# Kernel optimization log

Measured on AMD Instinct MI355X. Metric: run time of the kernel, lower is better.

Reference implementation:

```python
import jax, jax.numpy as jnp
import numpy as np

EPS = 1e-6


def _layernorm2d(x, w, b):
    # Normalize over channel dim (axis=1) per pixel; x: [B,C,H,W]
    mu = jnp.mean(x, axis=1, keepdims=True)
    var = jnp.var(x, axis=1, keepdims=True)
    xn = (x - mu) * jax.lax.rsqrt(var + EPS)
    return xn * w[None, :, None, None] + b[None, :, None, None]


def _conv1x1(x, w, b):
    # 1x1 conv == channel matmul; w: [Cout, Cin], x: [B,Cin,H,W]
    return jnp.einsum('oc,bchw->bohw', w, x) + b[None, :, None, None]


def setup_inputs() -> dict:
    key = jax.random.key(0)
    ks = jax.random.split(key, 8)
    B, C, H, W = 4, 64, 180, 320
    s = C ** -0.5  # keep projection weights at sane scale
    return {
        'x_l': jax.random.normal(ks[0], (B, C, H, W), jnp.float32),
        'x_r': jax.random.normal(ks[1], (B, C, H, W), jnp.float32),
        'ln_l_w': jnp.ones((C,), jnp.float32),
        'ln_l_b': jnp.zeros((C,), jnp.float32),
        'ln_r_w': jnp.ones((C,), jnp.float32),
        'ln_r_b': jnp.zeros((C,), jnp.float32),
        'wq_l': jax.random.normal(ks[2], (C, C), jnp.float32) * s,
        'bq_l': jnp.zeros((C,), jnp.float32),
        'wq_r': jax.random.normal(ks[3], (C, C), jnp.float32) * s,
        'bq_r': jnp.zeros((C,), jnp.float32),
        'wv_l': jax.random.normal(ks[4], (C, C), jnp.float32) * s,
        'bv_l': jnp.zeros((C,), jnp.float32),
        'wv_r': jax.random.normal(ks[5], (C, C), jnp.float32) * s,
        'bv_r': jnp.zeros((C,), jnp.float32),
        'beta': jax.random.normal(ks[6], (C,), jnp.float32) * 0.1,
        'gamma': jax.random.normal(ks[7], (C,), jnp.float32) * 0.1,
    }


def reference(x_l, x_r, ln_l_w, ln_l_b, ln_r_w, ln_r_b,
              wq_l, bq_l, wq_r, bq_r, wv_l, bv_l, wv_r, bv_r,
              beta, gamma):
    C = x_l.shape[1]
    scale = C ** -0.5
    # Q projections of LayerNorm'd inputs (Select stub == identity pass-through)
    Q_l = _conv1x1(_layernorm2d(x_l, ln_l_w, ln_l_b), wq_l, bq_l)  # [B,C,H,W]
    Q_r = _conv1x1(_layernorm2d(x_r, ln_r_w, ln_r_b), wq_r, bq_r)  # [B,C,H,W]
    V_l = _conv1x1(x_l, wv_l, bv_l)  # [B,C,H,W]
    V_r = _conv1x1(x_r, wv_r, bv_r)  # [B,C,H,W]
    # attention over width per row: [B,H,Wl,Wr]
    attn = jnp.einsum('bchw,bchv->bhwv', Q_l, Q_r) * scale
    # r -> l: softmax over Wr (last axis), contract with V_r
    F_r2l = jnp.einsum('bhwv,bchv->bchw', jax.nn.softmax(attn, axis=-1), V_r)
    # l -> r: softmax over Wl (axis=2 of attn), contract with V_l
    F_l2r = jnp.einsum('bhwv,bchw->bchv', jax.nn.softmax(attn, axis=2), V_l)
    out_l = x_l + F_r2l * beta[None, :, None, None]
    out_r = x_r + F_l2r * gamma[None, :, None, None]
    return (out_l, out_r)
```

## Files before the change

### kernel.cpp

```cpp
#include <hip/hip_runtime.h>


#define HWs  57600
#define CHWs 3686400
#define TOTs 14745600
#define RST  72
#define VST  328
#define PTS  36
#define NTH  768

typedef short bf16x8 __attribute__((ext_vector_type(8)));
typedef float f32x4  __attribute__((ext_vector_type(4)));
union FragU { uint4 q; unsigned short u[8]; bf16x8 v; };

__device__ __forceinline__ unsigned short f2bf(float f) {
  unsigned u = __float_as_uint(f);
  u += 0x7fffu + ((u >> 16) & 1u);
  return (unsigned short)(u >> 16);
}
__device__ __forceinline__ float bf2f(unsigned short s) {
  return __uint_as_float(((unsigned)s) << 16);
}
__device__ __forceinline__ unsigned fenc(float f) {
  unsigned u = __float_as_uint(f);
  return u ^ (0x80000000u | (unsigned)(-(int)(u >> 31)));
}
__device__ __forceinline__ float fdec(unsigned k) {
  return __uint_as_float(k ^ (0x80000000u | (unsigned)(-(int)((k >> 31) ^ 1u))));
}

__global__ __launch_bounds__(NTH, 3)
void sfam_kernel(
    const float* __restrict__ x_l, const float* __restrict__ x_r,
    const float* __restrict__ ln_l_w, const float* __restrict__ ln_l_b,
    const float* __restrict__ ln_r_w, const float* __restrict__ ln_r_b,
    const float* __restrict__ wq_l, const float* __restrict__ bq_l,
    const float* __restrict__ wq_r, const float* __restrict__ bq_r,
    const float* __restrict__ wv_l, const float* __restrict__ bv_l,
    const float* __restrict__ wv_r, const float* __restrict__ bv_r,
    const float* __restrict__ beta, const float* __restrict__ gamma,
    float* __restrict__ out)
{
  __shared__ __align__(16) unsigned short Rs[320*RST];
  __shared__ __align__(16) unsigned short Ks[320*RST];
  __shared__ __align__(16) unsigned short Vb[64*VST];
  __shared__ __align__(16) unsigned short Pt[12*16*PTS];
  __shared__ unsigned CMu[320];
  __shared__ float MU[640], RSd[640];
  __shared__ float c_arr[320];
  __shared__ float BB[128];

  const int bh = blockIdx.x;
  const int b = bh / 180, h = bh - b*180;
  const int base = b*CHWs + h*320;

  const int t = threadIdx.x;
  const int wave = t >> 6, lane = t & 63;
  const int p = lane & 15, g = lane >> 4;
  const int nwt = (wave < 8) ? 2 : 1;
  const int w0 = (wave < 8) ? wave*32 : 256 + (wave-8)*16;

  for (int w2 = t; w2 < 640; w2 += NTH) {
    const int side = (w2 >= 320);
    const int w = w2 - side*320;
    const float* xp = side ? x_r : x_l;
    unsigned short* dst = side ? Ks : Rs;
    float s0 = 0.f, q0 = 0.f, s1 = 0.f, q1 = 0.f;
    #pragma unroll
    for (int cb = 0; cb < 64; cb += 8) {
      FragU f;
      #pragma unroll
      for (int j = 0; j < 8; ++j) {
        const float v = xp[base + (cb+j)*HWs + w];
        if (cb < 32) { s0 += v; q0 += v*v; } else { s1 += v; q1 += v*v; }
        f.u[j] = f2bf(v);
      }
      *(uint4*)&dst[w*RST + cb] = f.q;
    }
    const float m  = (s0 + s1) * (1.f/64.f);
    const float vv = (q0 + q1) * (1.f/64.f) - m*m;
    MU[side*320 + w]  = m;
    RSd[side*320 + w] = rsqrtf(vv + 1e-6f);
  }
  if (t < 320) CMu[t] = 0u;
  if (t < 128) {
    const int o = t & 63;
    const float* wqp = (t < 64) ? wq_l : wq_r;
    const float* lwp = (t < 64) ? ln_l_w : ln_r_w;
    const float* lbp = (t < 64) ? ln_l_b : ln_r_b;
    const float* bqp = (t < 64) ? bq_l : bq_r;
    float s = bqp[o];
    for (int c = 0; c < 64; ++c) s += wqp[o*64+c]*lwp[c]*lbp[c];
    BB[t] = s;
  }
  __syncthreads();

  auto projV = [&](const float* wvp, const float* bvp, const unsigned short* src,
                   const float* mup, const float* rsp, bool inv) {
    bf16x8 bx[2][2];
    #pragma unroll
    for (int nt = 0; nt < 2; ++nt) if (nt < nwt) {
      const int w = w0 + nt*16 + p;
      const float mu = mup[w];
      const float sd = inv ? (1.0f / rsp[w]) : 0.f;
      #pragma unroll
      for (int kf = 0; kf < 2; ++kf) {
        FragU f; f.q = *(const uint4*)&src[w*RST + kf*32 + g*8];
        if (inv) {
          FragU rr;
          #pragma unroll
          for (int j = 0; j < 8; ++j) rr.u[j] = f2bf(bf2f(f.u[j])*sd + mu);
          bx[nt][kf] = rr.v;
        } else bx[nt][kf] = f.v;
      }
    }
    bf16x8 av[4][2];
    #pragma unroll
    for (int mt = 0; mt < 4; ++mt)
      #pragma unroll
      for (int kf = 0; kf < 2; ++kf) {
        FragU rr;
        #pragma unroll
        for (int j = 0; j < 8; ++j) rr.u[j] = f2bf(wvp[(mt*16+p)*64 + kf*32 + g*8 + j]);
        av[mt][kf] = rr.v;
      }
    f32x4 acc[4][2];
    #pragma unroll
    for (int mt = 0; mt < 4; ++mt)
      #pragma unroll
      for (int nt = 0; nt < 2; ++nt) acc[mt][nt] = (f32x4){0.f,0.f,0.f,0.f};
    #pragma unroll
    for (int mt = 0; mt < 4; ++mt)
      #pragma unroll
      for (int nt = 0; nt < 2; ++nt) if (nt < nwt)
        #pragma unroll
        for (int kf = 0; kf < 2; ++kf)
          acc[mt][nt] = __builtin_amdgcn_mfma_f32_16x16x32_bf16(av[mt][kf], bx[nt][kf], acc[mt][nt], 0,0,0);
    #pragma unroll
    for (int mt = 0; mt < 4; ++mt)
      #pragma unroll
      for (int nt = 0; nt < 2; ++nt) if (nt < nwt)
        #pragma unroll
        for (int r = 0; r < 4; ++r) {
          const int o = mt*16 + g*4 + r;
          Vb[o*VST + w0 + nt*16 + p] = f2bf(acc[mt][nt][r] + bvp[o]);
        }
  };

  projV(wv_l, bv_l, Rs, MU, RSd, false);

  float cR[2][4];
  {
    bf16x8 qa[2][2];
    #pragma unroll
    for (int wt = 0; wt < 2; ++wt) if (wt < nwt) {
      const int w = w0 + wt*16 + p;
      const float mu = MU[w], rs = RSd[w];
      #pragma unroll
      for (int kf = 0; kf < 2; ++kf) {
        FragU f; f.q = *(const uint4*)&Rs[w*RST + kf*32 + g*8];
        FragU rr;
        #pragma unroll
        for (int j = 0; j < 8; ++j) rr.u[j] = f2bf((bf2f(f.u[j]) - mu) * rs);
        qa[wt][kf] = rr.v;
      }
    }
    bf16x8 bw[4][2];
    #pragma unroll
    for (int ot = 0; ot < 4; ++ot)
      #pragma unroll
      for (int kf = 0; kf < 2; ++kf) {
        FragU rr;
        #pragma unroll
        for (int j = 0; j < 8; ++j) {
          const int c = kf*32 + g*8 + j;
          rr.u[j] = f2bf(wq_l[(ot*16+p)*64 + c] * ln_l_w[c]);
        }
        bw[ot][kf] = rr.v;
      }
    f32x4 qacc[2][4];
    #pragma unroll
    for (int wt = 0; wt < 2; ++wt)
      #pragma unroll
      for (int ot = 0; ot < 4; ++ot) qacc[wt][ot] = (f32x4){0.f,0.f,0.f,0.f};
    #pragma unroll
    for (int wt = 0; wt < 2; ++wt) if (wt < nwt)
      #pragma unroll
      for (int ot = 0; ot < 4; ++ot)
        #pragma unroll
        for (int kf = 0; kf < 2; ++kf)
          qacc[wt][ot] = __builtin_amdgcn_mfma_f32_16x16x32_bf16(qa[wt][kf], bw[ot][kf], qacc[wt][ot], 0,0,0);
    #pragma unroll
    for (int wt = 0; wt < 2; ++wt) {
      #pragma unroll
      for (int r = 0; r < 4; ++r) cR[wt][r] = 0.f;
      if (wt < nwt) {
        #pragma unroll
        for (int ot = 0; ot < 4; ++ot) {
          const float bl = BB[ot*16+p], br = BB[64 + ot*16+p];
          #pragma unroll
          for (int r = 0; r < 4; ++r) {
            const float qv = qacc[wt][ot][r] + bl;
            Rs[(w0 + wt*16 + g*4 + r)*RST + ot*16 + p] = f2bf(qv);
            cR[wt][r] += qv * br;
          }
        }
        #pragma unroll
        for (int r = 0; r < 4; ++r) {
          float cv = cR[wt][r];
          cv += __shfl_xor(cv, 1); cv += __shfl_xor(cv, 2);
          cv += __shfl_xor(cv, 4); cv += __shfl_xor(cv, 8);
          cv *= 0.125f;
          cR[wt][r] = cv;
          if (p == 0) c_arr[w0 + wt*16 + g*4 + r] = cv;
        }
      }
    }
  }

  {
    bf16x8 qla[2][2];
    #pragma unroll
    for (int wt = 0; wt < 2; ++wt) if (wt < nwt)
      #pragma unroll
      for (int kf = 0; kf < 2; ++kf) {
        FragU f; f.q = *(const uint4*)&Rs[(w0 + wt*16 + p)*RST + kf*32 + g*8];
        qla[wt][kf] = f.v;
      }
    bf16x8 bwt[4][2];
    #pragma unroll
    for (int ct = 0; ct < 4; ++ct) {
      const float lw = ln_r_w[ct*16 + p];
      #pragma unroll
      for (int kf = 0; kf < 2; ++kf) {
        FragU rr;
        #pragma unroll
        for (int j = 0; j < 8; ++j)
          rr.u[j] = f2bf(wq_r[(kf*32 + g*8 + j)*64 + ct*16 + p] * lw);
        bwt[ct][kf] = rr.v;
      }
    }
    f32x4 q2[2][4];
    #pragma unroll
    for (int wt = 0; wt < 2; ++wt)
      #pragma unroll
      for (int ct = 0; ct < 4; ++ct) q2[wt][ct] = (f32x4){0.f,0.f,0.f,0.f};
    #pragma unroll
    for (int wt = 0; wt < 2; ++wt) if (wt < nwt)
      #pragma unroll
      for (int ct = 0; ct < 4; ++ct)
        #pragma unroll
        for (int kf = 0; kf < 2; ++kf)
          q2[wt][ct] = __builtin_amdgcn_mfma_f32_16x16x32_bf16(qla[wt][kf], bwt[ct][kf], q2[wt][ct], 0,0,0);
    #pragma unroll
    for (int wt = 0; wt < 2; ++wt) if (wt < nwt)
      #pragma unroll
      for (int ct = 0; ct < 4; ++ct)
        #pragma unroll
        for (int r = 0; r < 4; ++r)
          Rs[(w0 + wt*16 + g*4 + r)*RST + ct*16 + p] = f2bf(q2[wt][ct][r] * 0.125f);
  }

  #pragma unroll
  for (int wt = 0; wt < 2; ++wt) if (wt < nwt) {
    const int w = w0 + wt*16 + p;
    const float mu = MU[320+w], rs = RSd[320+w];
    #pragma unroll
    for (int kf = 0; kf < 2; ++kf) {
      FragU f; f.q = *(const uint4*)&Ks[w*RST + kf*32 + g*8];
      FragU rr;
      #pragma unroll
      for (int j = 0; j < 8; ++j) rr.u[j] = f2bf((bf2f(f.u[j]) - mu) * rs);
      *(uint4*)&Ks[w*RST + kf*32 + g*8] = rr.q;
    }
  }
  __syncthreads();

  bf16x8 aq[2][2], ak[2][2];
  #pragma unroll
  for (int wt = 0; wt < 2; ++wt) if (wt < nwt)
    #pragma unroll
    for (int kf = 0; kf < 2; ++kf) {
      FragU f1; f1.q = *(const uint4*)&Rs[(w0 + wt*16 + p)*RST + kf*32 + g*8];
      aq[wt][kf] = f1.v;
      FragU f2; f2.q = *(const uint4*)&Ks[(w0 + wt*16 + p)*RST + kf*32 + g*8];
      ak[wt][kf] = f2.v;
    }

  float rm[2][4];
  #pragma unroll
  for (int wt = 0; wt < 2; ++wt)
    #pragma unroll
    for (int r = 0; r < 4; ++r) rm[wt][r] = -3.0e38f;
  for (int ch = 0; ch < 5; ++ch) {
    const int k0 = ch*64;
    bf16x8 bq[4][2];
    #pragma unroll
    for (int vt = 0; vt < 4; ++vt)
      #pragma unroll
      for (int kf = 0; kf < 2; ++kf) {
        FragU f; f.q = *(const uint4*)&Ks[(k0 + vt*16 + p)*RST + kf*32 + g*8];
        bq[vt][kf] = f.v;
      }
    f32x4 sacc[2][4];
    #pragma unroll
    for (int wt = 0; wt < 2; ++wt)
      #pragma unroll
      for (int vt = 0; vt < 4; ++vt) sacc[wt][vt] = (f32x4){0.f,0.f,0.f,0.f};
    #pragma unroll
    for (int wt = 0; wt < 2; ++wt) if (wt < nwt)
      #pragma unroll
      for (int vt = 0; vt < 4; ++vt)
        #pragma unroll
        for (int kf = 0; kf < 2; ++kf)
          sacc[wt][vt] = __builtin_amdgcn_mfma_f32_16x16x32_bf16(aq[wt][kf], bq[vt][kf], sacc[wt][vt], 0,0,0);
    #pragma unroll
    for (int wt = 0; wt < 2; ++wt) if (wt < nwt) {
      #pragma unroll
      for (int r = 0; r < 4; ++r) {
        float m4 = fmaxf(fmaxf(sacc[wt][0][r], sacc[wt][1][r]),
                         fmaxf(sacc[wt][2][r], sacc[wt][3][r])) + cR[wt][r];
        m4 = fmaxf(m4, __shfl_xor(m4, 1)); m4 = fmaxf(m4, __shfl_xor(m4, 2));
        m4 = fmaxf(m4, __shfl_xor(m4, 4)); m4 = fmaxf(m4, __shfl_xor(m4, 8));
        rm[wt][r] = fmaxf(rm[wt][r], m4);
      }
    }
    #pragma unroll
    for (int vt = 0; vt < 4; ++vt) {
      float cp = -3.0e38f;
      #pragma unroll
      for (int wt = 0; wt < 2; ++wt) if (wt < nwt)
        #pragma unroll
        for (int r = 0; r < 4; ++r) cp = fmaxf(cp, sacc[wt][vt][r] + cR[wt][r]);
      cp = fmaxf(cp, __shfl_xor(cp, 16));
      cp = fmaxf(cp, __shfl_xor(cp, 32));
      if (g == 0) atomicMax(&CMu[k0 + vt*16 + p], fenc(cp));
    }
  }
  __syncthreads();

  float ls[2][4];
  f32x4 oacc[2][4];
  auto attn_pass = [&](bf16x8 (&A)[2][2], const unsigned short* Bsrc,
                       float (&mx)[2][4], bool colc) {
    for (int ch = 0; ch < 5; ++ch) {
      const int k0 = ch*64;
      bf16x8 bq[4][2];
      #pragma unroll
      for (int vt = 0; vt < 4; ++vt)
        #pragma unroll
        for (int kf = 0; kf < 2; ++kf) {
          FragU f; f.q = *(const uint4*)&Bsrc[(k0 + vt*16 + p)*RST + kf*32 + g*8];
          bq[vt][kf] = f.v;
        }
      float cc4[4];
      #pragma unroll
      for (int vt = 0; vt < 4; ++vt) cc4[vt] = colc ? c_arr[k0 + vt*16 + p] : 0.f;
      f32x4 sacc[2][4];
      #pragma unroll
      for (int wt = 0; wt < 2; ++wt)
        #pragma unroll
        for (int vt = 0; vt < 4; ++vt) sacc[wt][vt] = (f32x4){0.f,0.f,0.f,0.f};
      #pragma unroll
      for (int wt = 0; wt < 2; ++wt) if (wt < nwt)
        #pragma unroll
        for (int vt = 0; vt < 4; ++vt)
          #pragma unroll
          for (int kf = 0; kf < 2; ++kf)
            sacc[wt][vt] = __builtin_amdgcn_mfma_f32_16x16x32_bf16(A[wt][kf], bq[vt][kf], sacc[wt][vt], 0,0,0);
      #pragma unroll
      for (int wt = 0; wt < 2; ++wt) if (wt < nwt) {
        #pragma unroll
        for (int r = 0; r < 4; ++r) {
          const float rc = colc ? 0.f : cR[wt][r];
          float rsum = 0.f;
          #pragma unroll
          for (int vt = 0; vt < 4; ++vt) {
            const float e = __expf(sacc[wt][vt][r] + rc + cc4[vt] - mx[wt][r]);
            sacc[wt][vt][r] = e; rsum += e;
          }
          rsum += __shfl_xor(rsum, 1); rsum += __shfl_xor(rsum, 2);
          rsum += __shfl_xor(rsum, 4); rsum += __shfl_xor(rsum, 8);
          ls[wt][r] += rsum;
        }
      }
      bf16x8 bvv[2][4];
      #pragma unroll
      for (int kf = 0; kf < 2; ++kf)
        #pragma unroll
        for (int ot = 0; ot < 4; ++ot) {
          FragU f; f.q = *(const uint4*)&Vb[(ot*16+p)*VST + k0 + kf*32 + g*8];
          bvv[kf][ot] = f.v;
        }
      unsigned short* ptw = &Pt[wave*16*PTS];
      #pragma unroll
      for (int wt = 0; wt < 2; ++wt) if (wt < nwt) {
        #pragma unroll
        for (int kf = 0; kf < 2; ++kf) {
          #pragma unroll
          for (int vh = 0; vh < 2; ++vh) {
            const int vt2 = kf*2 + vh;
            #pragma unroll
            for (int r = 0; r < 4; ++r)
              ptw[(g*4 + r)*PTS + vh*16 + p] = f2bf(sacc[wt][vt2][r]);
          }
          FragU fa; fa.q = *(const uint4*)&ptw[p*PTS + g*8];
          #pragma unroll
          for (int ot = 0; ot < 4; ++ot)
            oacc[wt][ot] = __builtin_amdgcn_mfma_f32_16x16x32_bf16(fa.v, bvv[kf][ot], oacc[wt][ot], 0,0,0);
        }
      }
    }
  };

  float cmR[2][4];
  #pragma unroll
  for (int wt = 0; wt < 2; ++wt)
    #pragma unroll
    for (int r = 0; r < 4; ++r) {
      cmR[wt][r] = (wt < nwt) ? fdec(CMu[w0 + wt*16 + g*4 + r]) : 0.f;
      ls[wt][r] = 0.f;
    }
  #pragma unroll
  for (int wt = 0; wt < 2; ++wt)
    #pragma unroll
    for (int ot = 0; ot < 4; ++ot) oacc[wt][ot] = (f32x4){0.f,0.f,0.f,0.f};
  attn_pass(ak, Rs, cmR, true);
  __syncthreads();

  #pragma unroll
  for (int wt = 0; wt < 2; ++wt) if (wt < nwt)
    #pragma unroll
    for (int r = 0; r < 4; ++r) {
      const float inv = 1.0f / ls[wt][r];
      #pragma unroll
      for (int ot = 0; ot < 4; ++ot)
        Rs[(w0 + wt*16 + g*4 + r)*RST + ot*16 + p] = f2bf(oacc[wt][ot][r] * inv);
    }

  projV(wv_r, bv_r, Ks, MU+320, RSd+320, true);
  __syncthreads();

  #pragma unroll
  for (int wt = 0; wt < 2; ++wt)
    #pragma unroll
    for (int r = 0; r < 4; ++r) ls[wt][r] = 0.f;
  #pragma unroll
  for (int wt = 0; wt < 2; ++wt)
    #pragma unroll
    for (int ot = 0; ot < 4; ++ot) oacc[wt][ot] = (f32x4){0.f,0.f,0.f,0.f};
  attn_pass(aq, Ks, rm, false);
  __syncthreads();

  #pragma unroll
  for (int wt = 0; wt < 2; ++wt) if (wt < nwt)
    #pragma unroll
    for (int r = 0; r < 4; ++r) {
      const float inv = 1.0f / ls[wt][r];
      #pragma unroll
      for (int ot = 0; ot < 4; ++ot)
        Ks[(w0 + wt*16 + g*4 + r)*RST + ot*16 + p] = f2bf(oacc[wt][ot][r] * inv);
    }
  __syncthreads();

  for (int w2 = t; w2 < 640; w2 += NTH) {
    const int side = (w2 >= 320);
    const int w = w2 - side*320;
    const float* xs = side ? x_r : x_l;
    const unsigned short* Osrc = side ? Rs : Ks;
    const float* sc = side ? gamma : beta;
    float* op = out + (side ? TOTs : 0);
    #pragma unroll
    for (int cb = 0; cb < 64; cb += 8) {
      FragU f; f.q = *(const uint4*)&Osrc[w*RST + cb];
      #pragma unroll
      for (int j = 0; j < 8; ++j) {
        const int cc = cb + j;
        const int gi = base + cc*HWs + w;
        op[gi] = xs[gi] + sc[cc] * bf2f(f.u[j]);
      }
    }
  }
}

extern "C" void kernel_launch(void* const* d_in, const int* in_sizes, int n_in,
                              void* d_out, int out_size, void* d_ws, size_t ws_size,
                              hipStream_t stream) {
  (void)in_sizes; (void)n_in; (void)d_ws; (void)ws_size; (void)out_size;
  sfam_kernel<<<dim3(720), dim3(NTH), 0, stream>>>(
      (const float*)d_in[0],  (const float*)d_in[1],
      (const float*)d_in[2],  (const float*)d_in[3],
      (const float*)d_in[4],  (const float*)d_in[5],
      (const float*)d_in[6],  (const float*)d_in[7],
      (const float*)d_in[8],  (const float*)d_in[9],
      (const float*)d_in[10], (const float*)d_in[11],
      (const float*)d_in[12], (const float*)d_in[13],
      (const float*)d_in[14], (const float*)d_in[15],
      (float*)d_out);
}
```

Baseline: 465.2 us.

## Restructure projection and attention loops to cut register pressure, relax launch bounds

Splits the weight-fragment loads and MFMAs in the V and Q projections per output tile so fewer fragments stay live at once. The score-max and attention passes now work on 32-column half chunks, keep per-lane partial row sums and maxima, and run the cross-lane shuffle reductions once at the end instead of once per chunk. The ak fragment load moves later to shorten its live range. Launch bounds drop from 3 to 2 blocks per CU, which gives each thread more registers to avoid spills but may lower occupancy.

```diff
diff --git a/kernel.cpp b/kernel.cpp
--- a/kernel.cpp
+++ b/kernel.cpp
@@ -29,7 +29,7 @@
   return __uint_as_float(k ^ (0x80000000u | (unsigned)(-(int)((k >> 31) ^ 1u))));
 }
 
-__global__ __launch_bounds__(NTH, 3)
+__global__ __launch_bounds__(NTH, 2)
 void sfam_kernel(
     const float* __restrict__ x_l, const float* __restrict__ x_r,
     const float* __restrict__ ln_l_w, const float* __restrict__ ln_l_b,
@@ -114,37 +114,32 @@
         } else bx[nt][kf] = f.v;
       }
     }
-    bf16x8 av[4][2];
-    #pragma unroll
-    for (int mt = 0; mt < 4; ++mt)
+    #pragma unroll
+    for (int mt = 0; mt < 4; ++mt) {
+      bf16x8 av2[2];
       #pragma unroll
       for (int kf = 0; kf < 2; ++kf) {
         FragU rr;
         #pragma unroll
         for (int j = 0; j < 8; ++j) rr.u[j] = f2bf(wvp[(mt*16+p)*64 + kf*32 + g*8 + j]);
-        av[mt][kf] = rr.v;
-      }
-    f32x4 acc[4][2];
-    #pragma unroll
-    for (int mt = 0; mt < 4; ++mt)
-      #pragma unroll
-      for (int nt = 0; nt < 2; ++nt) acc[mt][nt] = (f32x4){0.f,0.f,0.f,0.f};
-    #pragma unroll
-    for (int mt = 0; mt < 4; ++mt)
+        av2[kf] = rr.v;
+      }
+      f32x4 acc2[2];
+      #pragma unroll
+      for (int nt = 0; nt < 2; ++nt) acc2[nt] = (f32x4){0.f,0.f,0.f,0.f};
       #pragma unroll
       for (int nt = 0; nt < 2; ++nt) if (nt < nwt)
         #pragma unroll
         for (int kf = 0; kf < 2; ++kf)
-          acc[mt][nt] = __builtin_amdgcn_mfma_f32_16x16x32_bf16(av[mt][kf], bx[nt][kf], acc[mt][nt], 0,0,0);
-    #pragma unroll
-    for (int mt = 0; mt < 4; ++mt)
+          acc2[nt] = __builtin_amdgcn_mfma_f32_16x16x32_bf16(av2[kf], bx[nt][kf], acc2[nt], 0,0,0);
       #pragma unroll
       for (int nt = 0; nt < 2; ++nt) if (nt < nwt)
         #pragma unroll
         for (int r = 0; r < 4; ++r) {
           const int o = mt*16 + g*4 + r;
-          Vb[o*VST + w0 + nt*16 + p] = f2bf(acc[mt][nt][r] + bvp[o]);
-        }
+          Vb[o*VST + w0 + nt*16 + p] = f2bf(acc2[nt][r] + bvp[o]);
+        }
+    }
   };
 
   projV(wv_l, bv_l, Rs, MU, RSd, false);
@@ -165,9 +160,14 @@
         qa[wt][kf] = rr.v;
       }
     }
-    bf16x8 bw[4][2];
-    #pragma unroll
-    for (int ot = 0; ot < 4; ++ot)
+    f32x4 qacc[2][4];
+    #pragma unroll
+    for (int wt = 0; wt < 2; ++wt)
+      #pragma unroll
+      for (int ot = 0; ot < 4; ++ot) qacc[wt][ot] = (f32x4){0.f,0.f,0.f,0.f};
+    #pragma unroll
+    for (int ot = 0; ot < 4; ++ot) {
+      bf16x8 bw2[2];
       #pragma unroll
       for (int kf = 0; kf < 2; ++kf) {
         FragU rr;
@@ -176,20 +176,14 @@
           const int c = kf*32 + g*8 + j;
           rr.u[j] = f2bf(wq_l[(ot*16+p)*64 + c] * ln_l_w[c]);
         }
-        bw[ot][kf] = rr.v;
-      }
-    f32x4 qacc[2][4];
-    #pragma unroll
-    for (int wt = 0; wt < 2; ++wt)
-      #pragma unroll
-      for (int ot = 0; ot < 4; ++ot) qacc[wt][ot] = (f32x4){0.f,0.f,0.f,0.f};
-    #pragma unroll
-    for (int wt = 0; wt < 2; ++wt) if (wt < nwt)
-      #pragma unroll
-      for (int ot = 0; ot < 4; ++ot)
+        bw2[kf] = rr.v;
+      }
+      #pragma unroll
+      for (int wt = 0; wt < 2; ++wt) if (wt < nwt)
         #pragma unroll
         for (int kf = 0; kf < 2; ++kf)
-          qacc[wt][ot] = __builtin_amdgcn_mfma_f32_16x16x32_bf16(qa[wt][kf], bw[ot][kf], qacc[wt][ot], 0,0,0);
+          qacc[wt][ot] = __builtin_amdgcn_mfma_f32_16x16x32_bf16(qa[wt][kf], bw2[kf], qacc[wt][ot], 0,0,0);
+    }
     #pragma unroll
     for (int wt = 0; wt < 2; ++wt) {
       #pragma unroll
@@ -227,31 +221,29 @@
         FragU f; f.q = *(const uint4*)&Rs[(w0 + wt*16 + p)*RST + kf*32 + g*8];
         qla[wt][kf] = f.v;
       }
-    bf16x8 bwt[4][2];
+    f32x4 q2[2][4];
+    #pragma unroll
+    for (int wt = 0; wt < 2; ++wt)
+      #pragma unroll
+      for (int ct = 0; ct < 4; ++ct) q2[wt][ct] = (f32x4){0.f,0.f,0.f,0.f};
     #pragma unroll
     for (int ct = 0; ct < 4; ++ct) {
       const float lw = ln_r_w[ct*16 + p];
+      bf16x8 bwt2[2];
       #pragma unroll
       for (int kf = 0; kf < 2; ++kf) {
         FragU rr;
         #pragma unroll
         for (int j = 0; j < 8; ++j)
           rr.u[j] = f2bf(wq_r[(kf*32 + g*8 + j)*64 + ct*16 + p] * lw);
-        bwt[ct][kf] = rr.v;
-      }
-    }
-    f32x4 q2[2][4];
-    #pragma unroll
-    for (int wt = 0; wt < 2; ++wt)
-      #pragma unroll
-      for (int ct = 0; ct < 4; ++ct) q2[wt][ct] = (f32x4){0.f,0.f,0.f,0.f};
-    #pragma unroll
-    for (int wt = 0; wt < 2; ++wt) if (wt < nwt)
-      #pragma unroll
-      for (int ct = 0; ct < 4; ++ct)
+        bwt2[kf] = rr.v;
+      }
+      #pragma unroll
+      for (int wt = 0; wt < 2; ++wt) if (wt < nwt)
         #pragma unroll
         for (int kf = 0; kf < 2; ++kf)
-          q2[wt][ct] = __builtin_amdgcn_mfma_f32_16x16x32_bf16(qla[wt][kf], bwt[ct][kf], q2[wt][ct], 0,0,0);
+          q2[wt][ct] = __builtin_amdgcn_mfma_f32_16x16x32_bf16(qla[wt][kf], bwt2[kf], q2[wt][ct], 0,0,0);
+    }
     #pragma unroll
     for (int wt = 0; wt < 2; ++wt) if (wt < nwt)
       #pragma unroll
@@ -276,151 +268,161 @@
   }
   __syncthreads();
 
-  bf16x8 aq[2][2], ak[2][2];
+  bf16x8 aq[2][2];
   #pragma unroll
   for (int wt = 0; wt < 2; ++wt) if (wt < nwt)
     #pragma unroll
     for (int kf = 0; kf < 2; ++kf) {
       FragU f1; f1.q = *(const uint4*)&Rs[(w0 + wt*16 + p)*RST + kf*32 + g*8];
       aq[wt][kf] = f1.v;
-      FragU f2; f2.q = *(const uint4*)&Ks[(w0 + wt*16 + p)*RST + kf*32 + g*8];
-      ak[wt][kf] = f2.v;
-    }
-
-  float rm[2][4];
+    }
+
+  float rmx[2][4];
   #pragma unroll
   for (int wt = 0; wt < 2; ++wt)
     #pragma unroll
-    for (int r = 0; r < 4; ++r) rm[wt][r] = -3.0e38f;
+    for (int r = 0; r < 4; ++r) rmx[wt][r] = -3.0e38f;
   for (int ch = 0; ch < 5; ++ch) {
     const int k0 = ch*64;
-    bf16x8 bq[4][2];
-    #pragma unroll
-    for (int vt = 0; vt < 4; ++vt)
-      #pragma unroll
-      for (int kf = 0; kf < 2; ++kf) {
-        FragU f; f.q = *(const uint4*)&Ks[(k0 + vt*16 + p)*RST + kf*32 + g*8];
-        bq[vt][kf] = f.v;
-      }
-    f32x4 sacc[2][4];
-    #pragma unroll
-    for (int wt = 0; wt < 2; ++wt)
-      #pragma unroll
-      for (int vt = 0; vt < 4; ++vt) sacc[wt][vt] = (f32x4){0.f,0.f,0.f,0.f};
-    #pragma unroll
-    for (int wt = 0; wt < 2; ++wt) if (wt < nwt)
-      #pragma unroll
-      for (int vt = 0; vt < 4; ++vt)
-        #pragma unroll
-        for (int kf = 0; kf < 2; ++kf)
-          sacc[wt][vt] = __builtin_amdgcn_mfma_f32_16x16x32_bf16(aq[wt][kf], bq[vt][kf], sacc[wt][vt], 0,0,0);
-    #pragma unroll
-    for (int wt = 0; wt < 2; ++wt) if (wt < nwt) {
+    #pragma unroll
+    for (int vt = 0; vt < 4; ++vt) {
+      FragU f0, f1;
+      f0.q = *(const uint4*)&Ks[(k0 + vt*16 + p)*RST + g*8];
+      f1.q = *(const uint4*)&Ks[(k0 + vt*16 + p)*RST + 32 + g*8];
+      f32x4 s0 = (f32x4){0.f,0.f,0.f,0.f};
+      s0 = __builtin_amdgcn_mfma_f32_16x16x32_bf16(aq[0][0], f0.v, s0, 0,0,0);
+      s0 = __builtin_amdgcn_mfma_f32_16x16x32_bf16(aq[0][1], f1.v, s0, 0,0,0);
+      float cp = -3.0e38f;
       #pragma unroll
       for (int r = 0; r < 4; ++r) {
-        float m4 = fmaxf(fmaxf(sacc[wt][0][r], sacc[wt][1][r]),
-                         fmaxf(sacc[wt][2][r], sacc[wt][3][r])) + cR[wt][r];
-        m4 = fmaxf(m4, __shfl_xor(m4, 1)); m4 = fmaxf(m4, __shfl_xor(m4, 2));
-        m4 = fmaxf(m4, __shfl_xor(m4, 4)); m4 = fmaxf(m4, __shfl_xor(m4, 8));
-        rm[wt][r] = fmaxf(rm[wt][r], m4);
-      }
-    }
-    #pragma unroll
-    for (int vt = 0; vt < 4; ++vt) {
-      float cp = -3.0e38f;
-      #pragma unroll
-      for (int wt = 0; wt < 2; ++wt) if (wt < nwt)
-        #pragma unroll
-        for (int r = 0; r < 4; ++r) cp = fmaxf(cp, sacc[wt][vt][r] + cR[wt][r]);
+        const float v0 = s0[r] + cR[0][r];
+        rmx[0][r] = fmaxf(rmx[0][r], v0);
+        cp = fmaxf(cp, v0);
+      }
+      if (nwt > 1) {
+        f32x4 s1 = (f32x4){0.f,0.f,0.f,0.f};
+        s1 = __builtin_amdgcn_mfma_f32_16x16x32_bf16(aq[1][0], f0.v, s1, 0,0,0);
+        s1 = __builtin_amdgcn_mfma_f32_16x16x32_bf16(aq[1][1], f1.v, s1, 0,0,0);
+        #pragma unroll
+        for (int r = 0; r < 4; ++r) {
+          const float v1 = s1[r] + cR[1][r];
+          rmx[1][r] = fmaxf(rmx[1][r], v1);
+          cp = fmaxf(cp, v1);
+        }
+      }
       cp = fmaxf(cp, __shfl_xor(cp, 16));
       cp = fmaxf(cp, __shfl_xor(cp, 32));
       if (g == 0) atomicMax(&CMu[k0 + vt*16 + p], fenc(cp));
     }
   }
+  float rm[2][4];
+  #pragma unroll
+  for (int wt = 0; wt < 2; ++wt)
+    #pragma unroll
+    for (int r = 0; r < 4; ++r) {
+      float m = rmx[wt][r];
+      m = fmaxf(m, __shfl_xor(m, 1)); m = fmaxf(m, __shfl_xor(m, 2));
+      m = fmaxf(m, __shfl_xor(m, 4)); m = fmaxf(m, __shfl_xor(m, 8));
+      rm[wt][r] = m;
+    }
   __syncthreads();
 
   float ls[2][4];
   f32x4 oacc[2][4];
   auto attn_pass = [&](bf16x8 (&A)[2][2], const unsigned short* Bsrc,
                        float (&mx)[2][4], bool colc) {
+    float rsa[2][4];
+    #pragma unroll
+    for (int wt = 0; wt < 2; ++wt)
+      #pragma unroll
+      for (int r = 0; r < 4; ++r) rsa[wt][r] = 0.f;
+    unsigned short* ptw = &Pt[wave*16*PTS];
     for (int ch = 0; ch < 5; ++ch) {
       const int k0 = ch*64;
-      bf16x8 bq[4][2];
-      #pragma unroll
-      for (int vt = 0; vt < 4; ++vt)
-        #pragma unroll
-        for (int kf = 0; kf < 2; ++kf) {
-          FragU f; f.q = *(const uint4*)&Bsrc[(k0 + vt*16 + p)*RST + kf*32 + g*8];
-          bq[vt][kf] = f.v;
-        }
-      float cc4[4];
-      #pragma unroll
-      for (int vt = 0; vt < 4; ++vt) cc4[vt] = colc ? c_arr[k0 + vt*16 + p] : 0.f;
-      f32x4 sacc[2][4];
-      #pragma unroll
-      for (int wt = 0; wt < 2; ++wt)
-        #pragma unroll
-        for (int vt = 0; vt < 4; ++vt) sacc[wt][vt] = (f32x4){0.f,0.f,0.f,0.f};
-      #pragma unroll
-      for (int wt = 0; wt < 2; ++wt) if (wt < nwt)
-        #pragma unroll
-        for (int vt = 0; vt < 4; ++vt)
-          #pragma unroll
-          for (int kf = 0; kf < 2; ++kf)
-            sacc[wt][vt] = __builtin_amdgcn_mfma_f32_16x16x32_bf16(A[wt][kf], bq[vt][kf], sacc[wt][vt], 0,0,0);
-      #pragma unroll
-      for (int wt = 0; wt < 2; ++wt) if (wt < nwt) {
-        #pragma unroll
-        for (int r = 0; r < 4; ++r) {
-          const float rc = colc ? 0.f : cR[wt][r];
-          float rsum = 0.f;
-          #pragma unroll
-          for (int vt = 0; vt < 4; ++vt) {
-            const float e = __expf(sacc[wt][vt][r] + rc + cc4[vt] - mx[wt][r]);
-            sacc[wt][vt][r] = e; rsum += e;
+      #pragma unroll
+      for (int pvk = 0; pvk < 2; ++pvk) {
+        bf16x8 bq2[2][2];
+        #pragma unroll
+        for (int vh = 0; vh < 2; ++vh)
+          #pragma unroll
+          for (int kf = 0; kf < 2; ++kf) {
+            FragU f; f.q = *(const uint4*)&Bsrc[(k0 + (pvk*2+vh)*16 + p)*RST + kf*32 + g*8];
+            bq2[vh][kf] = f.v;
           }
-          rsum += __shfl_xor(rsum, 1); rsum += __shfl_xor(rsum, 2);
-          rsum += __shfl_xor(rsum, 4); rsum += __shfl_xor(rsum, 8);
-          ls[wt][r] += rsum;
-        }
-      }
-      bf16x8 bvv[2][4];
-      #pragma unroll
-      for (int kf = 0; kf < 2; ++kf)
+        float cc2[2];
+        #pragma unroll
+        for (int vh = 0; vh < 2; ++vh)
+          cc2[vh] = colc ? c_arr[k0 + (pvk*2+vh)*16 + p] : 0.f;
+        f32x4 sa[2][2];
+        #pragma unroll
+        for (int wt = 0; wt < 2; ++wt)
+          #pragma unroll
+          for (int vh = 0; vh < 2; ++vh) sa[wt][vh] = (f32x4){0.f,0.f,0.f,0.f};
+        #pragma unroll
+        for (int wt = 0; wt < 2; ++wt) if (wt < nwt)
+          #pragma unroll
+          for (int vh = 0; vh < 2; ++vh)
+            #pragma unroll
+            for (int kf = 0; kf < 2; ++kf)
+              sa[wt][vh] = __builtin_amdgcn_mfma_f32_16x16x32_bf16(A[wt][kf], bq2[vh][kf], sa[wt][vh], 0,0,0);
+        #pragma unroll
+        for (int wt = 0; wt < 2; ++wt) if (wt < nwt) {
+          #pragma unroll
+          for (int r = 0; r < 4; ++r) {
+            const float rc = colc ? 0.f : cR[wt][r];
+            #pragma unroll
+            for (int vh = 0; vh < 2; ++vh) {
+              const float e = __expf(sa[wt][vh][r] + rc + cc2[vh] - mx[wt][r]);
+              sa[wt][vh][r] = e;
+              rsa[wt][r] += e;
+            }
+          }
+        }
+        bf16x8 bvv[4];
         #pragma unroll
         for (int ot = 0; ot < 4; ++ot) {
-          FragU f; f.q = *(const uint4*)&Vb[(ot*16+p)*VST + k0 + kf*32 + g*8];
-          bvv[kf][ot] = f.v;
-        }
-      unsigned short* ptw = &Pt[wave*16*PTS];
-      #pragma unroll
-      for (int wt = 0; wt < 2; ++wt) if (wt < nwt) {
-        #pragma unroll
-        for (int kf = 0; kf < 2; ++kf) {
-          #pragma unroll
-          for (int vh = 0; vh < 2; ++vh) {
-            const int vt2 = kf*2 + vh;
+          FragU f; f.q = *(const uint4*)&Vb[(ot*16+p)*VST + k0 + pvk*32 + g*8];
+          bvv[ot] = f.v;
+        }
+        #pragma unroll
+        for (int wt = 0; wt < 2; ++wt) if (wt < nwt) {
+          #pragma unroll
+          for (int vh = 0; vh < 2; ++vh)
             #pragma unroll
             for (int r = 0; r < 4; ++r)
-              ptw[(g*4 + r)*PTS + vh*16 + p] = f2bf(sacc[wt][vt2][r]);
-          }
+              ptw[(g*4 + r)*PTS + vh*16 + p] = f2bf(sa[wt][vh][r]);
           FragU fa; fa.q = *(const uint4*)&ptw[p*PTS + g*8];
           #pragma unroll
           for (int ot = 0; ot < 4; ++ot)
-            oacc[wt][ot] = __builtin_amdgcn_mfma_f32_16x16x32_bf16(fa.v, bvv[kf][ot], oacc[wt][ot], 0,0,0);
-        }
-      }
-    }
+            oacc[wt][ot] = __builtin_amdgcn_mfma_f32_16x16x32_bf16(fa.v, bvv[ot], oacc[wt][ot], 0,0,0);
+        }
+      }
+    }
+    #pragma unroll
+    for (int wt = 0; wt < 2; ++wt)
+      #pragma unroll
+      for (int r = 0; r < 4; ++r) {
+        float s = rsa[wt][r];
+        s += __shfl_xor(s, 1); s += __shfl_xor(s, 2);
+        s += __shfl_xor(s, 4); s += __shfl_xor(s, 8);
+        ls[wt][r] = s;
+      }
   };
 
+  bf16x8 ak[2][2];
+  #pragma unroll
+  for (int wt = 0; wt < 2; ++wt) if (wt < nwt)
+    #pragma unroll
+    for (int kf = 0; kf < 2; ++kf) {
+      FragU f2; f2.q = *(const uint4*)&Ks[(w0 + wt*16 + p)*RST + kf*32 + g*8];
+      ak[wt][kf] = f2.v;
+    }
   float cmR[2][4];
   #pragma unroll
   for (int wt = 0; wt < 2; ++wt)
     #pragma unroll
-    for (int r = 0; r < 4; ++r) {
+    for (int r = 0; r < 4; ++r)
       cmR[wt][r] = (wt < nwt) ? fdec(CMu[w0 + wt*16 + g*4 + r]) : 0.f;
-      ls[wt][r] = 0.f;
-    }
   #pragma unroll
   for (int wt = 0; wt < 2; ++wt)
     #pragma unroll
@@ -441,10 +443,6 @@
   projV(wv_r, bv_r, Ks, MU+320, RSd+320, true);
   __syncthreads();
 
-  #pragma unroll
-  for (int wt = 0; wt < 2; ++wt)
-    #pragma unroll
-    for (int r = 0; r < 4; ++r) ls[wt][r] = 0.f;
   #pragma unroll
   for (int wt = 0; wt < 2; ++wt)
     #pragma unroll
```

New measurement: 426.5 us. -8.3%, faster.
